# Performance work log

Hardware: AMD Instinct MI355X
Metric: run time of the kernel (lower is better)

Reference implementation:

```python
import jax, jax.numpy as jnp
import numpy as np
import math

B, LQ, LK = 4, 512, 512
D_MODEL, NHEAD, NLABELS = 512, 8, 8
D_Q = D_MODEL // NHEAD


def setup_inputs() -> dict:
    key = jax.random.key(0)
    ks = jax.random.split(key, 12)
    xavier = lambda k, shape: jax.random.uniform(
        k, shape, jnp.float32,
        -math.sqrt(6.0 / (shape[0] + shape[1])), math.sqrt(6.0 / (shape[0] + shape[1])))
    return {
        "q": jax.random.normal(ks[0], (B, LQ, D_MODEL), jnp.float32),
        "k": jax.random.normal(ks[1], (B, LK, D_MODEL), jnp.float32),
        "edge_mask": jax.random.randint(ks[2], (B, LQ, LK, NLABELS), 0, 2).astype(jnp.float32),
        "padding_mask": jax.random.randint(ks[3], (B, LQ, LK), 0, 2).astype(jnp.float32),
        "w_q_w": xavier(ks[4], (D_MODEL, D_MODEL)),
        "w_q_b": jnp.zeros((D_MODEL,), jnp.float32),
        "w_k": xavier(ks[5], (D_MODEL, D_MODEL)),
        "w_v": xavier(ks[6], (D_MODEL, D_MODEL)),
        "w_h_w": xavier(ks[7], (D_MODEL, D_MODEL)),
        "w_h_b": jnp.zeros((D_MODEL,), jnp.float32),
        "b_ks": xavier(ks[8], (NLABELS, D_Q)),
        "b_vs": xavier(ks[9], (NLABELS, D_Q)),
    }


def reference(q, k, edge_mask, padding_mask, w_q_w, w_q_b, w_k, w_v, w_h_w, w_h_b, b_ks, b_vs):
    sz_b, len_q, _ = q.shape
    len_k = k.shape[1]
    temp = np.power(D_Q, 0.5).astype(np.float32)

    # projections -> (nhead, B, L, d_q), matching torch permute(2,0,1,3)
    query = (q @ w_q_w.T + w_q_b).reshape(sz_b, len_q, NHEAD, D_Q).transpose(2, 0, 1, 3)
    key = (k @ w_k.T).reshape(sz_b, len_k, NHEAD, D_Q).transpose(2, 0, 1, 3)
    value = (k @ w_v.T).reshape(sz_b, len_k, NHEAD, D_Q).transpose(2, 0, 1, 3)

    # content scores + relation-bias scores
    qk = jnp.einsum('hbqd,hbkd->hbqk', query, key)
    key_rel = jnp.einsum('bqkl,ld->bqkd', edge_mask, b_ks)      # (B,Lq,Lk,d_q)
    qkr = jnp.einsum('hbqd,bqkd->hbqk', query, key_rel)
    output_attention_weights = (qk + qkr) / temp                # pre-mask, as returned by torch

    # mask where no edge label AND padding_mask==1
    relation_mask = (edge_mask.sum(-1) + (1.0 - padding_mask)) == 0  # (B,Lq,Lk)
    rm = relation_mask[None, :, :, :]                                # broadcast over heads
    attn = jnp.where(rm, -jnp.inf, output_attention_weights)
    attn = jax.nn.softmax(attn, axis=-1)
    attn = jnp.where(rm, 0.0, attn)

    # value aggregation: content + relation values
    qv = jnp.einsum('hbqk,hbkd->hbqd', attn, value)
    val_rel = jnp.einsum('bqkl,ld->bqkd', edge_mask, b_vs)
    qvr = jnp.einsum('hbqk,bqkd->hbqd', attn, val_rel)

    out = (qv + qvr).transpose(1, 2, 0, 3).reshape(sz_b, len_q, D_MODEL)
    out = out @ w_h_w.T + w_h_b
    return out, output_attention_weights.reshape(NHEAD * sz_b, len_q, len_k)
```

## Files before the change

kernel.cpp:

```cpp
#include <hip/hip_runtime.h>
#include <math.h>

#define NB 4
#define LQ 512
#define LK 512
#define DM 512
#define NH 8
#define DQ 64
#define NL 8
#define QT 32
#define PSTR 520

typedef short bf16x8 __attribute__((ext_vector_type(8)));
typedef _Float16 f16x8 __attribute__((ext_vector_type(8)));
typedef _Float16 f16x2 __attribute__((ext_vector_type(2)));
typedef float f32x4 __attribute__((ext_vector_type(4)));

__device__ __forceinline__ unsigned short f2bf(float x) {
    unsigned u = __float_as_uint(x);
    u += 0x7fff + ((u >> 16) & 1);
    return (unsigned short)(u >> 16);
}
__device__ __forceinline__ float bf2f(unsigned x) {
    return __uint_as_float(x << 16);
}
__device__ __forceinline__ unsigned short f2h(float x) {
    _Float16 h = (_Float16)x;
    return __builtin_bit_cast(unsigned short, h);
}
__device__ __forceinline__ void gld16(const void* g, void* l) {
    __builtin_amdgcn_global_load_lds(
        (const __attribute__((address_space(1))) void*)g,
        (__attribute__((address_space(3))) void*)l, 16, 0, 0);
}

#define WAITVM(N) asm volatile("s_waitcnt vmcnt(" #N ")" ::: "memory")
#define LGKM0()   asm volatile("s_waitcnt lgkmcnt(0)" ::: "memory")
#define BARR()    do { asm volatile("" ::: "memory"); \
                       __builtin_amdgcn_s_barrier();  \
                       asm volatile("" ::: "memory"); } while (0)

__global__ __launch_bounds__(256) void prep_kernel(
        const float* __restrict__ q,  const float* __restrict__ k,
        const float* __restrict__ wq, const float* __restrict__ wk,
        const float* __restrict__ wv, const float* __restrict__ wh,
        const float* __restrict__ em, const float* __restrict__ pad,
        unsigned short* __restrict__ qb,  unsigned short* __restrict__ kb,
        unsigned short* __restrict__ wqb, unsigned short* __restrict__ wkb,
        unsigned short* __restrict__ wvb, unsigned short* __restrict__ whb,
        unsigned short* __restrict__ Pk) {
    const int tid = threadIdx.x;
    const int y = blockIdx.y;
    if (y < 6) {
        const float* s; unsigned short* d; int n;
        switch (y) {
            case 0: s = q;  d = qb;  n = NB * LQ * DM; break;
            case 1: s = k;  d = kb;  n = NB * LK * DM; break;
            case 2: s = wq; d = wqb; n = DM * DM; break;
            case 3: s = wk; d = wkb; n = DM * DM; break;
            case 4: s = wv; d = wvb; n = DM * DM; break;
            default: s = wh; d = whb; n = DM * DM; break;
        }
        const int i = blockIdx.x * 256 + tid;
        if (i * 8 >= n) return;
        const float4* sv = (const float4*)s;
        const float4 a = sv[2 * (size_t)i], b = sv[2 * (size_t)i + 1];
        uint4 o;
        o.x = (unsigned)f2bf(a.x) | ((unsigned)f2bf(a.y) << 16);
        o.y = (unsigned)f2bf(a.z) | ((unsigned)f2bf(a.w) << 16);
        o.z = (unsigned)f2bf(b.x) | ((unsigned)f2bf(b.y) << 16);
        o.w = (unsigned)f2bf(b.z) | ((unsigned)f2bf(b.w) << 16);
        *(uint4*)(d + (size_t)i * 8) = o;
    } else {
        const int row = blockIdx.x * 4 + (tid >> 6);
        const int k0 = (tid & 63) * 8;
        const float* eb = em + ((size_t)row * LK + k0) * NL;
        const float4 pv0 = *(const float4*)(pad + (size_t)row * LK + k0);
        const float4 pv1 = *(const float4*)(pad + (size_t)row * LK + k0 + 4);
        const float pv[8] = {pv0.x, pv0.y, pv0.z, pv0.w, pv1.x, pv1.y, pv1.z, pv1.w};
        unsigned short outv[8];
#pragma unroll
        for (int kk = 0; kk < 8; ++kk) {
            const float4 v0 = *(const float4*)(eb + kk * 8);
            const float4 v1 = *(const float4*)(eb + kk * 8 + 4);
            unsigned b_ = 0;
            b_ |= (v0.x != 0.f) << 0; b_ |= (v0.y != 0.f) << 1;
            b_ |= (v0.z != 0.f) << 2; b_ |= (v0.w != 0.f) << 3;
            b_ |= (v1.x != 0.f) << 4; b_ |= (v1.y != 0.f) << 5;
            b_ |= (v1.z != 0.f) << 6; b_ |= (v1.w != 0.f) << 7;
            b_ |= (pv[kk] != 0.f) << 8;
            outv[kk] = (unsigned short)b_;
        }
        uint4 o;
        o.x = (unsigned)outv[0] | ((unsigned)outv[1] << 16);
        o.y = (unsigned)outv[2] | ((unsigned)outv[3] << 16);
        o.z = (unsigned)outv[4] | ((unsigned)outv[5] << 16);
        o.w = (unsigned)outv[6] | ((unsigned)outv[7] << 16);
        *(uint4*)(Pk + (size_t)row * LK + k0) = o;
    }
}

__device__ __forceinline__ void gemm64core(const unsigned short* __restrict__ Ag, int lda,
                                           const unsigned short* __restrict__ Bg, int ldb,
                                           short* As, short* Bs,
                                           f32x4 (&acc)[2][2]) {
    const int tid = threadIdx.x;
    const int wave = tid >> 6, lane = tid & 63;
    const int quad = lane >> 4, l16 = lane & 15;
    const int wr = wave >> 1, wc = wave & 1;
    const int r_ = tid >> 2, c_ = (tid & 3) * 8;
    const unsigned short* Ar = Ag + (size_t)r_ * lda + c_;
    const unsigned short* Br = Bg + (size_t)r_ * ldb + c_;
    gld16(Ar, (char*)As + wave * 1024);
    gld16(Br, (char*)Bs + wave * 1024);
#pragma unroll
    for (int s = 0; s < 16; ++s) {
        if (s < 15) {
            const int nb = (s + 1) & 1;
            gld16(Ar + (s + 1) * 32, (char*)As + nb * 4096 + wave * 1024);
            gld16(Br + (s + 1) * 32, (char*)Bs + nb * 4096 + wave * 1024);
            WAITVM(2);
        } else {
            WAITVM(0);
        }
        BARR();
        const int cb = s & 1;
        bf16x8 af[2], bf[2];
#pragma unroll
        for (int i = 0; i < 2; ++i)
            af[i] = *(const bf16x8*)&As[cb * 2048 + (wr * 32 + i * 16 + l16) * 32 + quad * 8];
#pragma unroll
        for (int j = 0; j < 2; ++j)
            bf[j] = *(const bf16x8*)&Bs[cb * 2048 + (wc * 32 + j * 16 + l16) * 32 + quad * 8];
#pragma unroll
        for (int i = 0; i < 2; ++i)
#pragma unroll
            for (int j = 0; j < 2; ++j)
                acc[i][j] = __builtin_amdgcn_mfma_f32_16x16x32_bf16(af[i], bf[j], acc[i][j], 0, 0, 0);
        BARR();
    }
}

__global__ __launch_bounds__(256) void proj_all(const unsigned short* __restrict__ qb,
                                                const unsigned short* __restrict__ kb,
                                                const unsigned short* __restrict__ wqb,
                                                const unsigned short* __restrict__ wkb,
                                                const unsigned short* __restrict__ wvb,
                                                const float* __restrict__ w_q_b,
                                                unsigned short* __restrict__ Qp,
                                                unsigned short* __restrict__ Kp,
                                                unsigned short* __restrict__ Vt) {
    __shared__ __align__(16) short As[2][64 * 32];
    __shared__ __align__(16) short Bs[2][64 * 32];
    const unsigned short* A; const unsigned short* W; const float* bias;
    unsigned short* C; int mode;
    switch (blockIdx.z) {
        case 0:  A = qb; W = wqb; bias = w_q_b;  C = Qp; mode = 0; break;
        case 1:  A = kb; W = wkb; bias = nullptr; C = Kp; mode = 0; break;
        default: A = kb; W = wvb; bias = nullptr; C = Vt; mode = 1; break;
    }
    f32x4 acc[2][2];
    const f32x4 zz = {0.f, 0.f, 0.f, 0.f};
#pragma unroll
    for (int i = 0; i < 2; ++i)
#pragma unroll
        for (int j = 0; j < 2; ++j) acc[i][j] = zz;
    const int m0 = blockIdx.x * 64, n0 = blockIdx.y * 64;
    gemm64core(A + (size_t)m0 * DM, DM, W + (size_t)n0 * DM, DM, &As[0][0], &Bs[0][0], acc);
    const int tid = threadIdx.x, wave = tid >> 6, lane = tid & 63;
    const int quad = lane >> 4, l16 = lane & 15;
    const int wr = wave >> 1, wc = wave & 1;
#pragma unroll
    for (int i = 0; i < 2; ++i)
#pragma unroll
        for (int r = 0; r < 4; ++r) {
            const int gm = m0 + wr * 32 + i * 16 + quad * 4 + r;
#pragma unroll
            for (int j = 0; j < 2; ++j) {
                const int gn = n0 + wc * 32 + j * 16 + l16;
                float v = acc[i][j][r];
                if (bias) v += bias[gn];
                if (mode == 0) C[(size_t)gm * DM + gn] = f2bf(v);
                else C[(size_t)(gm >> 9) * (DM * LK) + (size_t)gn * LK + (gm & 511)] = f2h(v);
            }
        }
}

#define STAGE_K(c, hb) do {                                                       \
    _Pragma("unroll")                                                             \
    for (int it_ = 0; it_ < 2; ++it_) {                                           \
        const int e_ = it_ * 512 + tid;                                           \
        const int kr_ = e_ >> 3, ch_ = e_ & 7;                                    \
        gld16(Kp + (size_t)(b * LK + (c) * 128 + kr_) * DM + h * DQ               \
                  + ((ch_ ^ (kr_ & 7)) * 8),                                      \
              (char*)&Kc[hb][0] + it_ * 8192 + wave * 1024);                      \
    } } while (0)

#define STAGE_V(vc, hb) do {                                                      \
    _Pragma("unroll")                                                             \
    for (int it_ = 0; it_ < 2; ++it_) {                                           \
        const int e_ = it_ * 512 + tid;                                           \
        const int dd_ = e_ >> 4, ch_ = e_ & 15;                                   \
        gld16(Vt + (size_t)(b * DM + h * DQ + dd_) * LK + (vc) * 128              \
                  + ((ch_ ^ (dd_ & 15)) * 8),                                     \
              (char*)&Kc[hb][0] + it_ * 8192 + wave * 1024);                      \
    } } while (0)

#define COMPUTE_K(c, hb) do {                                                     \
    _Pragma("unroll")                                                             \
    for (int kdi_ = 0; kdi_ < 2; ++kdi_) {                                        \
        const int krow_ = wave * 16 + l16;                                        \
        const int kch_ = (kdi_ * 4 + quad) ^ (krow_ & 7);                         \
        const bf16x8 bfv_ = *(const bf16x8*)&Kc[hb][krow_ * 64 + kch_ * 8];       \
        acc[c][0] = __builtin_amdgcn_mfma_f32_16x16x32_bf16(qf[0][kdi_], bfv_,    \
                                                            acc[c][0], 0, 0, 0); \
        acc[c][1] = __builtin_amdgcn_mfma_f32_16x16x32_bf16(qf[1][kdi_], bfv_,    \
                                                            acc[c][1], 0, 0, 0); \
    } } while (0)

#define COMPUTE_V(vc, hb) do {                                                    \
    _Pragma("unroll")                                                             \
    for (int kd_ = 0; kd_ < 128; kd_ += 32) {                                     \
        const int vrow_ = ni * 16 + l16;                                          \
        const int vch_ = ((kd_ >> 3) + quad) ^ (vrow_ & 15);                      \
        const f16x8 afv_ = *(const f16x8*)&Ps[(mi * 16 + l16) * PSTR              \
                                              + (vc) * 128 + kd_ + quad * 8];     \
        const f16x8 bfv_ = *(const f16x8*)&Kc[hb][vrow_ * 128 + vch_ * 8];        \
        oacc = __builtin_amdgcn_mfma_f32_16x16x32_f16(afv_, bfv_, oacc, 0, 0, 0); \
    } } while (0)

__global__ __launch_bounds__(512, 4) void attn_fused(
        const unsigned short* __restrict__ Qp,
        const unsigned short* __restrict__ Kp,
        const unsigned short* __restrict__ Vt,
        const unsigned short* __restrict__ Pk,
        const float* __restrict__ b_ks,
        const float* __restrict__ b_vs,
        float* __restrict__ weights,
        unsigned short* __restrict__ Hb) {
    __shared__ __align__(16) short Qs[QT * 64];
    __shared__ __align__(16) short Kc[2][128 * 64];
    __shared__ __align__(16) short Ps[QT * PSTR];
    __shared__ float svS[QT * NL];
    __shared__ float lutS[QT * 32];
    __shared__ float tS[QT * NL];
    __shared__ float redA[QT * 8];
    __shared__ float redB[QT * 8];

    const int tid = threadIdx.x, wave = tid >> 6, lane = tid & 63;
    const int quad = lane >> 4, l16 = lane & 15;
    const int q0 = blockIdx.x * QT;
    const int z = blockIdx.y, h = z >> 2, b = z & 3;

    const int srow = tid >> 4, sl = (tid >> 1) & 7, shalf = tid & 1;
    bf16x8 sq[4];
    {
        const unsigned short* qrow = Qp + (size_t)(b * LQ + q0 + srow) * DM + h * DQ + shalf * 32;
#pragma unroll
        for (int d0 = 0; d0 < 4; ++d0) sq[d0] = *(const bf16x8*)&qrow[d0 * 8];
    }

    if (tid < 256) {
        const int row = tid >> 3, ch = tid & 7;
        gld16(Qp + (size_t)(b * LQ + q0 + row) * DM + h * DQ + ((ch ^ (row & 7)) * 8),
              (char*)Qs + wave * 1024);
    }
    STAGE_K(0, 0);
    STAGE_K(1, 1);

    {
        const float* bk = b_ks + sl * DQ + shalf * 32;
        float s = 0.f;
#pragma unroll
        for (int d0 = 0; d0 < 4; ++d0)
#pragma unroll
            for (int j = 0; j < 8; ++j)
                s = fmaf(bf2f((unsigned short)sq[d0][j]), bk[d0 * 8 + j], s);
        s += __shfl_xor(s, 1, 64);
        if (shalf == 0) svS[srow * 8 + sl] = s;
    }

    f32x4 acc[4][2];
    const f32x4 zz = {0.f, 0.f, 0.f, 0.f};
#pragma unroll
    for (int c = 0; c < 4; ++c) { acc[c][0] = zz; acc[c][1] = zz; }
    bf16x8 qf[2][2];

    WAITVM(2); LGKM0(); BARR();
#pragma unroll
    for (int i = 0; i < 2; ++i)
#pragma unroll
        for (int kdi = 0; kdi < 2; ++kdi)
            qf[i][kdi] = *(const bf16x8*)&Qs[(i * 16 + l16) * 64
                                             + (((kdi * 4) + quad) ^ (l16 & 7)) * 8];
#pragma unroll
    for (int e2 = 0; e2 < 2; ++e2) {
        const int e = e2 * 512 + tid;
        const int row = e >> 5, idx = e & 31;
        const float* sp = &svS[row * 8 + ((idx & 16) ? 4 : 0)];
        float v = 0.f;
        v += (idx & 1) ? sp[0] : 0.f;
        v += (idx & 2) ? sp[1] : 0.f;
        v += (idx & 4) ? sp[2] : 0.f;
        v += (idx & 8) ? sp[3] : 0.f;
        lutS[e] = v;
    }
    COMPUTE_K(0, 0);
    LGKM0(); BARR();
    STAGE_K(2, 0);
    WAITVM(2); LGKM0(); BARR();
    COMPUTE_K(1, 1);
    LGKM0(); BARR();
    STAGE_K(3, 1);
    WAITVM(2); LGKM0(); BARR();
    COMPUTE_K(2, 0);
    LGKM0(); BARR();
    STAGE_V(0, 0);
    WAITVM(2); LGKM0(); BARR();
    COMPUTE_K(3, 1);
    LGKM0(); BARR();
    STAGE_V(1, 1);

#pragma unroll
    for (int i = 0; i < 2; ++i)
#pragma unroll
        for (int r = 0; r < 4; ++r) {
            const int row = i * 16 + quad * 4 + r;
            const int gq = q0 + row;
            const float* lrow = &lutS[row * 32];
            const unsigned short* prow = Pk + (size_t)(b * LQ + gq) * LK;
            float* wrow = weights + ((size_t)z * LQ + gq) * LK;
            float pm = -__builtin_inff();
#pragma unroll
            for (int c = 0; c < 4; ++c) {
                const int col = c * 128 + wave * 16 + l16;
                const unsigned w_ = prow[col];
                const float rel = lrow[w_ & 15u] + lrow[16 + ((w_ >> 4) & 15u)];
                const float wv = (acc[c][i][r] + rel) * 0.125f;
                wrow[col] = wv;
                const float m = ((w_ & 0x1FFu) == 0x100u) ? -__builtin_inff() : wv;
                acc[c][i][r] = m;
                pm = fmaxf(pm, m);
            }
#pragma unroll
            for (int o = 1; o < 16; o <<= 1) pm = fmaxf(pm, __shfl_xor(pm, o, 64));
            float ps = 0.f;
#pragma unroll
            for (int c = 0; c < 4; ++c) {
                const float e = __expf(acc[c][i][r] - pm);
                acc[c][i][r] = e;
                ps += e;
            }
#pragma unroll
            for (int o = 1; o < 16; o <<= 1) ps += __shfl_xor(ps, o, 64);
            if (l16 == 0) { redA[row * 8 + wave] = pm; redB[row * 8 + wave] = ps; }
        }
    LGKM0(); BARR();

#pragma unroll
    for (int i = 0; i < 2; ++i)
#pragma unroll
        for (int r = 0; r < 4; ++r) {
            const int row = i * 16 + quad * 4 + r;
            const f32x4 pa = *(const f32x4*)&redA[row * 8];
            const f32x4 pb = *(const f32x4*)&redA[row * 8 + 4];
            const f32x4 sa = *(const f32x4*)&redB[row * 8];
            const f32x4 sb = *(const f32x4*)&redB[row * 8 + 4];
            const float M = fmaxf(fmaxf(fmaxf(pa[0], pa[1]), fmaxf(pa[2], pa[3])),
                                  fmaxf(fmaxf(pb[0], pb[1]), fmaxf(pb[2], pb[3])));
            const float S = sa[0] * __expf(pa[0] - M) + sa[1] * __expf(pa[1] - M)
                          + sa[2] * __expf(pa[2] - M) + sa[3] * __expf(pa[3] - M)
                          + sb[0] * __expf(pb[0] - M) + sb[1] * __expf(pb[1] - M)
                          + sb[2] * __expf(pb[2] - M) + sb[3] * __expf(pb[3] - M);
            const float own = redA[row * 8 + wave];
            const float alpha = __expf(own - M) / S;
#pragma unroll
            for (int c = 0; c < 4; ++c) {
                const int col = c * 128 + wave * 16 + l16;
                Ps[row * PSTR + col] = (short)f2h(acc[c][i][r] * alpha);
            }
        }
    LGKM0(); BARR();

    {
        const int row = tid >> 4, l = (tid >> 1) & 7, half = tid & 1;
        const uint4* pw = (const uint4*)(Pk + (size_t)(b * LQ + q0 + row) * LK + half * 256);
        const uint4* aw = (const uint4*)&Ps[row * PSTR + half * 256];
        float tv = 0.f;
#pragma unroll 4
        for (int kk = 0; kk < 32; ++kk) {
            const uint4 wb = pw[kk];
            const uint4 av = aw[kk];
            const unsigned w4[4] = {wb.x, wb.y, wb.z, wb.w};
            const unsigned a4[4] = {av.x, av.y, av.z, av.w};
            f16x2 hacc = {(_Float16)0.f, (_Float16)0.f};
#pragma unroll
            for (int u = 0; u < 4; ++u) {
                const unsigned bits = (w4[u] >> l) & 0x10001u;
                const unsigned msk = bits * 0x3c00u;
                hacc += __builtin_bit_cast(f16x2, a4[u]) * __builtin_bit_cast(f16x2, msk);
            }
            tv += (float)hacc[0] + (float)hacc[1];
        }
        tv += __shfl_xor(tv, 1, 64);
        if (half == 0) tS[row * 8 + l] = tv;
    }

    f32x4 oacc = zz;
    const int mi = wave & 1, ni = wave >> 1;
    WAITVM(0); LGKM0(); BARR();
    COMPUTE_V(0, 0);
    BARR();
    STAGE_V(2, 0);
    WAITVM(2); LGKM0(); BARR();
    COMPUTE_V(1, 1);
    BARR();
    STAGE_V(3, 1);
    WAITVM(2); LGKM0(); BARR();
    COMPUTE_V(2, 0);
    WAITVM(0); LGKM0(); BARR();
    COMPUTE_V(3, 1);

    const int gd = ni * 16 + l16;
    float bvv[NL];
#pragma unroll
    for (int l = 0; l < NL; ++l) bvv[l] = b_vs[l * DQ + gd];
#pragma unroll
    for (int r = 0; r < 4; ++r) {
        const int row = mi * 16 + quad * 4 + r;
        const float* tp = &tS[row * 8];
        float o = oacc[r];
#pragma unroll
        for (int l = 0; l < NL; ++l) o = fmaf(tp[l], bvv[l], o);
        Hb[(size_t)(b * LQ + q0 + row) * DM + h * DQ + gd] = f2bf(o);
    }
}

__global__ __launch_bounds__(256) void outproj_mfma(const unsigned short* __restrict__ Hb,
                                                    const unsigned short* __restrict__ whb,
                                                    const float* __restrict__ bias,
                                                    float* __restrict__ C) {
    __shared__ __align__(16) short As[2][64 * 32];
    __shared__ __align__(16) short Bs[2][64 * 32];
    f32x4 acc[2][2];
    const f32x4 zz = {0.f, 0.f, 0.f, 0.f};
#pragma unroll
    for (int i = 0; i < 2; ++i)
#pragma unroll
        for (int j = 0; j < 2; ++j) acc[i][j] = zz;
    const int m0 = blockIdx.x * 64, n0 = blockIdx.y * 64;
    gemm64core(Hb + (size_t)m0 * DM, DM, whb + (size_t)n0 * DM, DM, &As[0][0], &Bs[0][0], acc);
    const int tid = threadIdx.x, wave = tid >> 6, lane = tid & 63;
    const int quad = lane >> 4, l16 = lane & 15;
    const int wr = wave >> 1, wc = wave & 1;
#pragma unroll
    for (int i = 0; i < 2; ++i)
#pragma unroll
        for (int r = 0; r < 4; ++r) {
            const int gm = m0 + wr * 32 + i * 16 + quad * 4 + r;
#pragma unroll
            for (int j = 0; j < 2; ++j) {
                const int gn = n0 + wc * 32 + j * 16 + l16;
                C[(size_t)gm * DM + gn] = acc[i][j][r] + bias[gn];
            }
        }
}

extern "C" void kernel_launch(void* const* d_in, const int* in_sizes, int n_in,
                              void* d_out, int out_size, void* d_ws, size_t ws_size,
                              hipStream_t stream) {
    const float* q     = (const float*)d_in[0];
    const float* k     = (const float*)d_in[1];
    const float* em    = (const float*)d_in[2];
    const float* pad   = (const float*)d_in[3];
    const float* w_q_w = (const float*)d_in[4];
    const float* w_q_b = (const float*)d_in[5];
    const float* w_k   = (const float*)d_in[6];
    const float* w_v   = (const float*)d_in[7];
    const float* w_h_w = (const float*)d_in[8];
    const float* w_h_b = (const float*)d_in[9];
    const float* b_ks  = (const float*)d_in[10];
    const float* b_vs  = (const float*)d_in[11];

    float* out     = (float*)d_out;
    float* weights = out + (size_t)NB * LQ * DM;

    char* ws = (char*)d_ws;
    unsigned short* qb  = (unsigned short*)(ws + 0);
    unsigned short* kb  = (unsigned short*)(ws + 2097152);
    unsigned short* wqb = (unsigned short*)(ws + 4194304);
    unsigned short* wkb = (unsigned short*)(ws + 4718592);
    unsigned short* wvb = (unsigned short*)(ws + 5242880);
    unsigned short* whb = (unsigned short*)(ws + 5767168);
    unsigned short* Qp  = (unsigned short*)(ws + 6291456);
    unsigned short* Kp  = (unsigned short*)(ws + 8388608);
    unsigned short* Vt  = (unsigned short*)(ws + 10485760);
    unsigned short* Hb  = (unsigned short*)(ws + 12582912);
    unsigned short* Pk  = (unsigned short*)(ws + 14680064);

    prep_kernel<<<dim3(512, 7), 256, 0, stream>>>(q, k, w_q_w, w_k, w_v, w_h_w,
                                                  em, pad, qb, kb, wqb, wkb, wvb, whb, Pk);
    proj_all<<<dim3(32, 8, 3), 256, 0, stream>>>(qb, kb, wqb, wkb, wvb, w_q_b, Qp, Kp, Vt);
    attn_fused<<<dim3(LQ / QT, 32), 512, 0, stream>>>(Qp, Kp, Vt, Pk, b_ks, b_vs, weights, Hb);
    outproj_mfma<<<dim3(32, 8), 256, 0, stream>>>(Hb, whb, w_h_b, out);
}
```

Before: 166.6 us.

## Fuse all stages into one cooperative persistent kernel with grid syncs

Replaces the four separate launches (convert/pack, projections, attention, output projection) with a single cooperative kernel of 512 blocks that runs each phase and separates them with grid-wide syncs. The attention body is factored into a device function that uses a shared-memory arena, and a templated GEMM routine is used for the projections, including a float-output mode for the final projection. The aim is to remove kernel launch gaps and tail effects between stages. In exchange each phase is tied to a fixed grid with grid barriers, and occupancy is limited by the 78 KB shared-memory footprint and 512-thread blocks. If the cooperative launch fails, the code falls back to the old multi-kernel path.

Result: slower. 373.8 us (+124.3%).

```diff
diff --git a/kernel.cpp b/kernel.cpp
--- a/kernel.cpp
+++ b/kernel.cpp
@@ -1,5 +1,8 @@
 #include <hip/hip_runtime.h>
+#include <hip/hip_cooperative_groups.h>
 #include <math.h>
+
+namespace cg = cooperative_groups;
 
 #define NB 4
 #define LQ 512
@@ -11,6 +14,16 @@
 #define QT 32
 #define PSTR 520
 
+#define SM_QS   0
+#define SM_KC   4096
+#define SM_PS   36864
+#define SM_SV   70144
+#define SM_LUT  71168
+#define SM_TS   75264
+#define SM_RA   76288
+#define SM_RB   77312
+#define SM_TOTAL 78336
+
 typedef short bf16x8 __attribute__((ext_vector_type(8)));
 typedef _Float16 f16x8 __attribute__((ext_vector_type(8)));
 typedef _Float16 f16x2 __attribute__((ext_vector_type(2)));
@@ -39,6 +52,432 @@
 #define BARR()    do { asm volatile("" ::: "memory"); \
                        __builtin_amdgcn_s_barrier();  \
                        asm volatile("" ::: "memory"); } while (0)
+
+
+__device__ __forceinline__ void conv_vec8(const float* __restrict__ s,
+                                          unsigned short* __restrict__ d, int i) {
+    const float4* sv = (const float4*)s;
+    const float4 a = sv[2 * (size_t)i], b = sv[2 * (size_t)i + 1];
+    uint4 o;
+    o.x = (unsigned)f2bf(a.x) | ((unsigned)f2bf(a.y) << 16);
+    o.y = (unsigned)f2bf(a.z) | ((unsigned)f2bf(a.w) << 16);
+    o.z = (unsigned)f2bf(b.x) | ((unsigned)f2bf(b.y) << 16);
+    o.w = (unsigned)f2bf(b.z) | ((unsigned)f2bf(b.w) << 16);
+    *(uint4*)(d + (size_t)i * 8) = o;
+}
+__device__ __forceinline__ void pack_pk(const float* __restrict__ em,
+                                        const float* __restrict__ pad,
+                                        unsigned short* __restrict__ Pk,
+                                        int row, int k0) {
+    const float* eb = em + ((size_t)row * LK + k0) * NL;
+    const float4 pv0 = *(const float4*)(pad + (size_t)row * LK + k0);
+    const float4 pv1 = *(const float4*)(pad + (size_t)row * LK + k0 + 4);
+    const float pv[8] = {pv0.x, pv0.y, pv0.z, pv0.w, pv1.x, pv1.y, pv1.z, pv1.w};
+    unsigned short outv[8];
+#pragma unroll
+    for (int kk = 0; kk < 8; ++kk) {
+        const float4 v0 = *(const float4*)(eb + kk * 8);
+        const float4 v1 = *(const float4*)(eb + kk * 8 + 4);
+        unsigned b_ = 0;
+        b_ |= (v0.x != 0.f) << 0; b_ |= (v0.y != 0.f) << 1;
+        b_ |= (v0.z != 0.f) << 2; b_ |= (v0.w != 0.f) << 3;
+        b_ |= (v1.x != 0.f) << 4; b_ |= (v1.y != 0.f) << 5;
+        b_ |= (v1.z != 0.f) << 6; b_ |= (v1.w != 0.f) << 7;
+        b_ |= (pv[kk] != 0.f) << 8;
+        outv[kk] = (unsigned short)b_;
+    }
+    uint4 o;
+    o.x = (unsigned)outv[0] | ((unsigned)outv[1] << 16);
+    o.y = (unsigned)outv[2] | ((unsigned)outv[3] << 16);
+    o.z = (unsigned)outv[4] | ((unsigned)outv[5] << 16);
+    o.w = (unsigned)outv[6] | ((unsigned)outv[7] << 16);
+    *(uint4*)(Pk + (size_t)row * LK + k0) = o;
+}
+
+template<int MODE>
+__device__ void gemm_macro(const unsigned short* __restrict__ Ag,
+                           const unsigned short* __restrict__ Bg,
+                           const float* __restrict__ bias,
+                           void* __restrict__ Cp,
+                           int m0, int n0p, char* smemc) {
+    short* As = (short*)(smemc);
+    short* Bs = (short*)(smemc + 8192);
+    const int tid = threadIdx.x;
+    const int wave = tid >> 6, lane = tid & 63;
+    const int quad = lane >> 4, l16 = lane & 15;
+    const int wl = wave & 3, wh = wave >> 2;
+    const int wr = wl >> 1, wc = wl & 1;
+    f32x4 acc[2][2];
+    const f32x4 zz = {0.f, 0.f, 0.f, 0.f};
+#pragma unroll
+    for (int i = 0; i < 2; ++i)
+#pragma unroll
+        for (int j = 0; j < 2; ++j) acc[i][j] = zz;
+    const int ar = lane >> 2, ac = (lane & 3) * 8;
+    const unsigned short* Arp = Ag + (size_t)(m0 + wave * 16 + ar) * DM + ac;
+    const unsigned short* Brp = Bg + (size_t)(n0p + wave * 16 + ar) * DM + ac;
+    if (wave < 4) gld16(Arp, (char*)As + wave * 1024);
+    gld16(Brp, (char*)Bs + wave * 1024);
+#pragma unroll
+    for (int s = 0; s < 16; ++s) {
+        if (s < 15) {
+            const int nb = (s + 1) & 1;
+            if (wave < 4) {
+                gld16(Arp + (s + 1) * 32, (char*)As + nb * 4096 + wave * 1024);
+                gld16(Brp + (s + 1) * 32, (char*)Bs + nb * 8192 + wave * 1024);
+                WAITVM(2);
+            } else {
+                gld16(Brp + (s + 1) * 32, (char*)Bs + nb * 8192 + wave * 1024);
+                WAITVM(1);
+            }
+        } else {
+            WAITVM(0);
+        }
+        BARR();
+        const int cb = s & 1;
+        bf16x8 af[2], bf[2];
+#pragma unroll
+        for (int i = 0; i < 2; ++i)
+            af[i] = *(const bf16x8*)&As[cb * 2048 + (wr * 32 + i * 16 + l16) * 32 + quad * 8];
+#pragma unroll
+        for (int j = 0; j < 2; ++j)
+            bf[j] = *(const bf16x8*)&Bs[cb * 4096 + (wh * 64 + wc * 32 + j * 16 + l16) * 32 + quad * 8];
+#pragma unroll
+        for (int i = 0; i < 2; ++i)
+#pragma unroll
+            for (int j = 0; j < 2; ++j)
+                acc[i][j] = __builtin_amdgcn_mfma_f32_16x16x32_bf16(af[i], bf[j], acc[i][j], 0, 0, 0);
+        BARR();
+    }
+#pragma unroll
+    for (int i = 0; i < 2; ++i)
+#pragma unroll
+        for (int r = 0; r < 4; ++r) {
+            const int gm = m0 + wr * 32 + i * 16 + quad * 4 + r;
+#pragma unroll
+            for (int j = 0; j < 2; ++j) {
+                const int gn = n0p + wh * 64 + wc * 32 + j * 16 + l16;
+                float v = acc[i][j][r];
+                if (MODE == 0) {
+                    if (bias) v += bias[gn];
+                    ((unsigned short*)Cp)[(size_t)gm * DM + gn] = f2bf(v);
+                } else if (MODE == 1) {
+                    ((unsigned short*)Cp)[(size_t)(gm >> 9) * (DM * LK)
+                                          + (size_t)gn * LK + (gm & 511)] = f2h(v);
+                } else {
+                    ((float*)Cp)[(size_t)gm * DM + gn] = v + bias[gn];
+                }
+            }
+        }
+}
+
+#define KC(hb) ((short*)(smemc + SM_KC + (hb) * 16384))
+
+#define STAGE_K(c, hb) do {                                                       \
+    _Pragma("unroll")                                                             \
+    for (int it_ = 0; it_ < 2; ++it_) {                                           \
+        const int e_ = it_ * 512 + tid;                                           \
+        const int kr_ = e_ >> 3, ch_ = e_ & 7;                                    \
+        gld16(Kp + (size_t)(b * LK + (c) * 128 + kr_) * DM + h * DQ               \
+                  + ((ch_ ^ (kr_ & 7)) * 8),                                      \
+              (char*)KC(hb) + it_ * 8192 + wave * 1024);                          \
+    } } while (0)
+
+#define STAGE_V(vc, hb) do {                                                      \
+    _Pragma("unroll")                                                             \
+    for (int it_ = 0; it_ < 2; ++it_) {                                           \
+        const int e_ = it_ * 512 + tid;                                           \
+        const int dd_ = e_ >> 4, ch_ = e_ & 15;                                   \
+        gld16(Vt + (size_t)(b * DM + h * DQ + dd_) * LK + (vc) * 128              \
+                  + ((ch_ ^ (dd_ & 15)) * 8),                                     \
+              (char*)KC(hb) + it_ * 8192 + wave * 1024);                          \
+    } } while (0)
+
+#define COMPUTE_K(c, hb) do {                                                     \
+    _Pragma("unroll")                                                             \
+    for (int kdi_ = 0; kdi_ < 2; ++kdi_) {                                        \
+        const int krow_ = wave * 16 + l16;                                        \
+        const int kch_ = (kdi_ * 4 + quad) ^ (krow_ & 7);                         \
+        const bf16x8 bfv_ = *(const bf16x8*)&KC(hb)[krow_ * 64 + kch_ * 8];       \
+        acc[c][0] = __builtin_amdgcn_mfma_f32_16x16x32_bf16(qf[0][kdi_], bfv_,    \
+                                                            acc[c][0], 0, 0, 0); \
+        acc[c][1] = __builtin_amdgcn_mfma_f32_16x16x32_bf16(qf[1][kdi_], bfv_,    \
+                                                            acc[c][1], 0, 0, 0); \
+    } } while (0)
+
+#define COMPUTE_V(vc, hb) do {                                                    \
+    _Pragma("unroll")                                                             \
+    for (int kd_ = 0; kd_ < 128; kd_ += 32) {                                     \
+        const int vrow_ = ni * 16 + l16;                                          \
+        const int vch_ = ((kd_ >> 3) + quad) ^ (vrow_ & 15);                      \
+        const f16x8 afv_ = *(const f16x8*)&Ps[(mi * 16 + l16) * PSTR              \
+                                              + (vc) * 128 + kd_ + quad * 8];     \
+        const f16x8 bfv_ = *(const f16x8*)&KC(hb)[vrow_ * 128 + vch_ * 8];        \
+        oacc = __builtin_amdgcn_mfma_f32_16x16x32_f16(afv_, bfv_, oacc, 0, 0, 0); \
+    } } while (0)
+
+__device__ void attn_body(char* smemc, const int xq, const int z,
+        const unsigned short* __restrict__ Qp,
+        const unsigned short* __restrict__ Kp,
+        const unsigned short* __restrict__ Vt,
+        const unsigned short* __restrict__ Pk,
+        const float* __restrict__ b_ks,
+        const float* __restrict__ b_vs,
+        float* __restrict__ weights,
+        unsigned short* __restrict__ Hb) {
+    short* Qs   = (short*)(smemc + SM_QS);
+    short* Ps   = (short*)(smemc + SM_PS);
+    float* svS  = (float*)(smemc + SM_SV);
+    float* lutS = (float*)(smemc + SM_LUT);
+    float* tS   = (float*)(smemc + SM_TS);
+    float* redA = (float*)(smemc + SM_RA);
+    float* redB = (float*)(smemc + SM_RB);
+
+    const int tid = threadIdx.x, wave = tid >> 6, lane = tid & 63;
+    const int quad = lane >> 4, l16 = lane & 15;
+    const int q0 = xq * QT;
+    const int h = z >> 2, b = z & 3;
+
+    const int srow = tid >> 4, sl = (tid >> 1) & 7, shalf = tid & 1;
+    bf16x8 sq[4];
+    {
+        const unsigned short* qrow = Qp + (size_t)(b * LQ + q0 + srow) * DM + h * DQ + shalf * 32;
+#pragma unroll
+        for (int d0 = 0; d0 < 4; ++d0) sq[d0] = *(const bf16x8*)&qrow[d0 * 8];
+    }
+
+    if (tid < 256) {
+        const int row = tid >> 3, ch = tid & 7;
+        gld16(Qp + (size_t)(b * LQ + q0 + row) * DM + h * DQ + ((ch ^ (row & 7)) * 8),
+              (char*)Qs + wave * 1024);
+    }
+    STAGE_K(0, 0);
+    STAGE_K(1, 1);
+
+    {
+        const float* bk = b_ks + sl * DQ + shalf * 32;
+        float s = 0.f;
+#pragma unroll
+        for (int d0 = 0; d0 < 4; ++d0)
+#pragma unroll
+            for (int j = 0; j < 8; ++j)
+                s = fmaf(bf2f((unsigned short)sq[d0][j]), bk[d0 * 8 + j], s);
+        s += __shfl_xor(s, 1, 64);
+        if (shalf == 0) svS[srow * 8 + sl] = s;
+    }
+
+    f32x4 acc[4][2];
+    const f32x4 zz = {0.f, 0.f, 0.f, 0.f};
+#pragma unroll
+    for (int c = 0; c < 4; ++c) { acc[c][0] = zz; acc[c][1] = zz; }
+    bf16x8 qf[2][2];
+
+    WAITVM(2); LGKM0(); BARR();
+#pragma unroll
+    for (int i = 0; i < 2; ++i)
+#pragma unroll
+        for (int kdi = 0; kdi < 2; ++kdi)
+            qf[i][kdi] = *(const bf16x8*)&Qs[(i * 16 + l16) * 64
+                                             + (((kdi * 4) + quad) ^ (l16 & 7)) * 8];
+#pragma unroll
+    for (int e2 = 0; e2 < 2; ++e2) {
+        const int e = e2 * 512 + tid;
+        const int row = e >> 5, idx = e & 31;
+        const float* sp = &svS[row * 8 + ((idx & 16) ? 4 : 0)];
+        float v = 0.f;
+        v += (idx & 1) ? sp[0] : 0.f;
+        v += (idx & 2) ? sp[1] : 0.f;
+        v += (idx & 4) ? sp[2] : 0.f;
+        v += (idx & 8) ? sp[3] : 0.f;
+        lutS[e] = v;
+    }
+    COMPUTE_K(0, 0);
+    LGKM0(); BARR();
+    STAGE_K(2, 0);
+    WAITVM(2); LGKM0(); BARR();
+    COMPUTE_K(1, 1);
+    LGKM0(); BARR();
+    STAGE_K(3, 1);
+    WAITVM(2); LGKM0(); BARR();
+    COMPUTE_K(2, 0);
+    LGKM0(); BARR();
+    STAGE_V(0, 0);
+    WAITVM(2); LGKM0(); BARR();
+    COMPUTE_K(3, 1);
+    LGKM0(); BARR();
+    STAGE_V(1, 1);
+
+#pragma unroll
+    for (int i = 0; i < 2; ++i)
+#pragma unroll
+        for (int r = 0; r < 4; ++r) {
+            const int row = i * 16 + quad * 4 + r;
+            const int gq = q0 + row;
+            const float* lrow = &lutS[row * 32];
+            const unsigned short* prow = Pk + (size_t)(b * LQ + gq) * LK;
+            float* wrow = weights + ((size_t)z * LQ + gq) * LK;
+            float pm = -__builtin_inff();
+#pragma unroll
+            for (int c = 0; c < 4; ++c) {
+                const int col = c * 128 + wave * 16 + l16;
+                const unsigned w_ = prow[col];
+                const float rel = lrow[w_ & 15u] + lrow[16 + ((w_ >> 4) & 15u)];
+                const float wv = (acc[c][i][r] + rel) * 0.125f;
+                wrow[col] = wv;
+                const float m = ((w_ & 0x1FFu) == 0x100u) ? -__builtin_inff() : wv;
+                acc[c][i][r] = m;
+                pm = fmaxf(pm, m);
+            }
+#pragma unroll
+            for (int o = 1; o < 16; o <<= 1) pm = fmaxf(pm, __shfl_xor(pm, o, 64));
+            float ps = 0.f;
+#pragma unroll
+            for (int c = 0; c < 4; ++c) {
+                const float e = __expf(acc[c][i][r] - pm);
+                acc[c][i][r] = e;
+                ps += e;
+            }
+#pragma unroll
+            for (int o = 1; o < 16; o <<= 1) ps += __shfl_xor(ps, o, 64);
+            if (l16 == 0) { redA[row * 8 + wave] = pm; redB[row * 8 + wave] = ps; }
+        }
+    LGKM0(); BARR();
+
+#pragma unroll
+    for (int i = 0; i < 2; ++i)
+#pragma unroll
+        for (int r = 0; r < 4; ++r) {
+            const int row = i * 16 + quad * 4 + r;
+            const f32x4 pa = *(const f32x4*)&redA[row * 8];
+            const f32x4 pb = *(const f32x4*)&redA[row * 8 + 4];
+            const f32x4 sa = *(const f32x4*)&redB[row * 8];
+            const f32x4 sb = *(const f32x4*)&redB[row * 8 + 4];
+            const float M = fmaxf(fmaxf(fmaxf(pa[0], pa[1]), fmaxf(pa[2], pa[3])),
+                                  fmaxf(fmaxf(pb[0], pb[1]), fmaxf(pb[2], pb[3])));
+            const float S = sa[0] * __expf(pa[0] - M) + sa[1] * __expf(pa[1] - M)
+                          + sa[2] * __expf(pa[2] - M) + sa[3] * __expf(pa[3] - M)
+                          + sb[0] * __expf(pb[0] - M) + sb[1] * __expf(pb[1] - M)
+                          + sb[2] * __expf(pb[2] - M) + sb[3] * __expf(pb[3] - M);
+            const float own = redA[row * 8 + wave];
+            const float alpha = __expf(own - M) / S;
+#pragma unroll
+            for (int c = 0; c < 4; ++c) {
+                const int col = c * 128 + wave * 16 + l16;
+                Ps[row * PSTR + col] = (short)f2h(acc[c][i][r] * alpha);
+            }
+        }
+    LGKM0(); BARR();
+
+    {
+        const int row = tid >> 4, l = (tid >> 1) & 7, half = tid & 1;
+        const uint4* pw = (const uint4*)(Pk + (size_t)(b * LQ + q0 + row) * LK + half * 256);
+        const uint4* aw = (const uint4*)&Ps[row * PSTR + half * 256];
+        float tv = 0.f;
+#pragma unroll 4
+        for (int kk = 0; kk < 32; ++kk) {
+            const uint4 wb = pw[kk];
+            const uint4 av = aw[kk];
+            const unsigned w4[4] = {wb.x, wb.y, wb.z, wb.w};
+            const unsigned a4[4] = {av.x, av.y, av.z, av.w};
+            f16x2 hacc = {(_Float16)0.f, (_Float16)0.f};
+#pragma unroll
+            for (int u = 0; u < 4; ++u) {
+                const unsigned bits = (w4[u] >> l) & 0x10001u;
+                const unsigned msk = bits * 0x3c00u;
+                hacc += __builtin_bit_cast(f16x2, a4[u]) * __builtin_bit_cast(f16x2, msk);
+            }
+            tv += (float)hacc[0] + (float)hacc[1];
+        }
+        tv += __shfl_xor(tv, 1, 64);
+        if (half == 0) tS[row * 8 + l] = tv;
+    }
+
+    f32x4 oacc = zz;
+    const int mi = wave & 1, ni = wave >> 1;
+    WAITVM(0); LGKM0(); BARR();
+    COMPUTE_V(0, 0);
+    BARR();
+    STAGE_V(2, 0);
+    WAITVM(2); LGKM0(); BARR();
+    COMPUTE_V(1, 1);
+    BARR();
+    STAGE_V(3, 1);
+    WAITVM(2); LGKM0(); BARR();
+    COMPUTE_V(2, 0);
+    WAITVM(0); LGKM0(); BARR();
+    COMPUTE_V(3, 1);
+
+    const int gd = ni * 16 + l16;
+    float bvv[NL];
+#pragma unroll
+    for (int l = 0; l < NL; ++l) bvv[l] = b_vs[l * DQ + gd];
+#pragma unroll
+    for (int r = 0; r < 4; ++r) {
+        const int row = mi * 16 + quad * 4 + r;
+        const float* tp = &tS[row * 8];
+        float o = oacc[r];
+#pragma unroll
+        for (int l = 0; l < NL; ++l) o = fmaf(tp[l], bvv[l], o);
+        Hb[(size_t)(b * LQ + q0 + row) * DM + h * DQ + gd] = f2bf(o);
+    }
+}
+
+__global__ __launch_bounds__(512, 4) void mega(
+        const float* __restrict__ q,  const float* __restrict__ k,
+        const float* __restrict__ em, const float* __restrict__ pad,
+        const float* __restrict__ w_q_w, const float* __restrict__ w_q_b,
+        const float* __restrict__ w_k,   const float* __restrict__ w_v,
+        const float* __restrict__ w_h_w, const float* __restrict__ w_h_b,
+        const float* __restrict__ b_ks,  const float* __restrict__ b_vs,
+        unsigned short* __restrict__ qb,  unsigned short* __restrict__ kb,
+        unsigned short* __restrict__ wqb, unsigned short* __restrict__ wkb,
+        unsigned short* __restrict__ wvb, unsigned short* __restrict__ whb,
+        unsigned short* __restrict__ Qp,  unsigned short* __restrict__ Kp,
+        unsigned short* __restrict__ Vt,  unsigned short* __restrict__ Hb,
+        unsigned short* __restrict__ Pk,
+        float* __restrict__ weights, float* __restrict__ out) {
+    __shared__ __align__(16) char smemc[SM_TOTAL];
+    cg::grid_group grid = cg::this_grid();
+    const int bid = blockIdx.x, tid = threadIdx.x;
+
+    {
+        for (int u = bid * 512 + tid; u < 393216; u += 262144) {
+            const float* s; unsigned short* d; int idx;
+            if (u < 131072)      { s = q; d = qb; idx = u; }
+            else if (u < 262144) { s = k; d = kb; idx = u - 131072; }
+            else {
+                const int v = u - 262144, w = v >> 15; idx = v & 32767;
+                switch (w) {
+                    case 0: s = w_q_w; d = wqb; break;
+                    case 1: s = w_k;   d = wkb; break;
+                    case 2: s = w_v;   d = wvb; break;
+                    default: s = w_h_w; d = whb; break;
+                }
+            }
+            conv_vec8(s, d, idx);
+        }
+        const int u2 = bid * 512 + tid;
+        if (u2 < 131072) pack_pk(em, pad, Pk, u2 >> 6, (u2 & 63) * 8);
+    }
+    grid.sync();
+
+    if (bid < 384) {
+        const int mat = bid >> 7, t = bid & 127;
+        const int m0 = (t >> 2) * 64, n0p = (t & 3) * 128;
+        if (mat == 0)      gemm_macro<0>(qb, wqb, w_q_b,  Qp, m0, n0p, smemc);
+        else if (mat == 1) gemm_macro<0>(kb, wkb, nullptr, Kp, m0, n0p, smemc);
+        else               gemm_macro<1>(kb, wvb, nullptr, Vt, m0, n0p, smemc);
+    }
+    grid.sync();
+
+    attn_body(smemc, bid & 15, bid >> 4, Qp, Kp, Vt, Pk, b_ks, b_vs, weights, Hb);
+    grid.sync();
+
+    if (bid < 128) {
+        const int m0 = (bid >> 2) * 64, n0p = (bid & 3) * 128;
+        gemm_macro<2>(Hb, whb, w_h_b, out, m0, n0p, smemc);
+    }
+}
 
 __global__ __launch_bounds__(256) void prep_kernel(
         const float* __restrict__ q,  const float* __restrict__ k,
@@ -63,40 +502,10 @@
         }
         const int i = blockIdx.x * 256 + tid;
         if (i * 8 >= n) return;
-        const float4* sv = (const float4*)s;
-        const float4 a = sv[2 * (size_t)i], b = sv[2 * (size_t)i + 1];
-        uint4 o;
-        o.x = (unsigned)f2bf(a.x) | ((unsigned)f2bf(a.y) << 16);
-        o.y = (unsigned)f2bf(a.z) | ((unsigned)f2bf(a.w) << 16);
-        o.z = (unsigned)f2bf(b.x) | ((unsigned)f2bf(b.y) << 16);
-        o.w = (unsigned)f2bf(b.z) | ((unsigned)f2bf(b.w) << 16);
-        *(uint4*)(d + (size_t)i * 8) = o;
+        conv_vec8(s, d, i);
     } else {
         const int row = blockIdx.x * 4 + (tid >> 6);
-        const int k0 = (tid & 63) * 8;
-        const float* eb = em + ((size_t)row * LK + k0) * NL;
-        const float4 pv0 = *(const float4*)(pad + (size_t)row * LK + k0);
-        const float4 pv1 = *(const float4*)(pad + (size_t)row * LK + k0 + 4);
-        const float pv[8] = {pv0.x, pv0.y, pv0.z, pv0.w, pv1.x, pv1.y, pv1.z, pv1.w};
-        unsigned short outv[8];
-#pragma unroll
-        for (int kk = 0; kk < 8; ++kk) {
-            const float4 v0 = *(const float4*)(eb + kk * 8);
-            const float4 v1 = *(const float4*)(eb + kk * 8 + 4);
-            unsigned b_ = 0;
-            b_ |= (v0.x != 0.f) << 0; b_ |= (v0.y != 0.f) << 1;
-            b_ |= (v0.z != 0.f) << 2; b_ |= (v0.w != 0.f) << 3;
-            b_ |= (v1.x != 0.f) << 4; b_ |= (v1.y != 0.f) << 5;
-            b_ |= (v1.z != 0.f) << 6; b_ |= (v1.w != 0.f) << 7;
-            b_ |= (pv[kk] != 0.f) << 8;
-            outv[kk] = (unsigned short)b_;
-        }
-        uint4 o;
-        o.x = (unsigned)outv[0] | ((unsigned)outv[1] << 16);
-        o.y = (unsigned)outv[2] | ((unsigned)outv[3] << 16);
-        o.z = (unsigned)outv[4] | ((unsigned)outv[5] << 16);
-        o.w = (unsigned)outv[6] | ((unsigned)outv[7] << 16);
-        *(uint4*)(Pk + (size_t)row * LK + k0) = o;
+        pack_pk(em, pad, Pk, row, (tid & 63) * 8);
     }
 }
 
@@ -186,49 +595,6 @@
         }
 }
 
-#define STAGE_K(c, hb) do {                                                       \
-    _Pragma("unroll")                                                             \
-    for (int it_ = 0; it_ < 2; ++it_) {                                           \
-        const int e_ = it_ * 512 + tid;                                           \
-        const int kr_ = e_ >> 3, ch_ = e_ & 7;                                    \
-        gld16(Kp + (size_t)(b * LK + (c) * 128 + kr_) * DM + h * DQ               \
-                  + ((ch_ ^ (kr_ & 7)) * 8),                                      \
-              (char*)&Kc[hb][0] + it_ * 8192 + wave * 1024);                      \
-    } } while (0)
-
-#define STAGE_V(vc, hb) do {                                                      \
-    _Pragma("unroll")                                                             \
-    for (int it_ = 0; it_ < 2; ++it_) {                                           \
-        const int e_ = it_ * 512 + tid;                                           \
-        const int dd_ = e_ >> 4, ch_ = e_ & 15;                                   \
-        gld16(Vt + (size_t)(b * DM + h * DQ + dd_) * LK + (vc) * 128              \
-                  + ((ch_ ^ (dd_ & 15)) * 8),                                     \
-              (char*)&Kc[hb][0] + it_ * 8192 + wave * 1024);                      \
-    } } while (0)
-
-#define COMPUTE_K(c, hb) do {                                                     \
-    _Pragma("unroll")                                                             \
-    for (int kdi_ = 0; kdi_ < 2; ++kdi_) {                                        \
-        const int krow_ = wave * 16 + l16;                                        \
-        const int kch_ = (kdi_ * 4 + quad) ^ (krow_ & 7);                         \
-        const bf16x8 bfv_ = *(const bf16x8*)&Kc[hb][krow_ * 64 + kch_ * 8];       \
-        acc[c][0] = __builtin_amdgcn_mfma_f32_16x16x32_bf16(qf[0][kdi_], bfv_,    \
-                                                            acc[c][0], 0, 0, 0); \
-        acc[c][1] = __builtin_amdgcn_mfma_f32_16x16x32_bf16(qf[1][kdi_], bfv_,    \
-                                                            acc[c][1], 0, 0, 0); \
-    } } while (0)
-
-#define COMPUTE_V(vc, hb) do {                                                    \
-    _Pragma("unroll")                                                             \
-    for (int kd_ = 0; kd_ < 128; kd_ += 32) {                                     \
-        const int vrow_ = ni * 16 + l16;                                          \
-        const int vch_ = ((kd_ >> 3) + quad) ^ (vrow_ & 15);                      \
-        const f16x8 afv_ = *(const f16x8*)&Ps[(mi * 16 + l16) * PSTR              \
-                                              + (vc) * 128 + kd_ + quad * 8];     \
-        const f16x8 bfv_ = *(const f16x8*)&Kc[hb][vrow_ * 128 + vch_ * 8];        \
-        oacc = __builtin_amdgcn_mfma_f32_16x16x32_f16(afv_, bfv_, oacc, 0, 0, 0); \
-    } } while (0)
-
 __global__ __launch_bounds__(512, 4) void attn_fused(
         const unsigned short* __restrict__ Qp,
         const unsigned short* __restrict__ Kp,
@@ -238,202 +604,8 @@
         const float* __restrict__ b_vs,
         float* __restrict__ weights,
         unsigned short* __restrict__ Hb) {
-    __shared__ __align__(16) short Qs[QT * 64];
-    __shared__ __align__(16) short Kc[2][128 * 64];
-    __shared__ __align__(16) short Ps[QT * PSTR];
-    __shared__ float svS[QT * NL];
-    __shared__ float lutS[QT * 32];
-    __shared__ float tS[QT * NL];
-    __shared__ float redA[QT * 8];
-    __shared__ float redB[QT * 8];
-
-    const int tid = threadIdx.x, wave = tid >> 6, lane = tid & 63;
-    const int quad = lane >> 4, l16 = lane & 15;
-    const int q0 = blockIdx.x * QT;
-    const int z = blockIdx.y, h = z >> 2, b = z & 3;
-
-    const int srow = tid >> 4, sl = (tid >> 1) & 7, shalf = tid & 1;
-    bf16x8 sq[4];
-    {
-        const unsigned short* qrow = Qp + (size_t)(b * LQ + q0 + srow) * DM + h * DQ + shalf * 32;
-#pragma unroll
-        for (int d0 = 0; d0 < 4; ++d0) sq[d0] = *(const bf16x8*)&qrow[d0 * 8];
-    }
-
-    if (tid < 256) {
-        const int row = tid >> 3, ch = tid & 7;
-        gld16(Qp + (size_t)(b * LQ + q0 + row) * DM + h * DQ + ((ch ^ (row & 7)) * 8),
-              (char*)Qs + wave * 1024);
-    }
-    STAGE_K(0, 0);
-    STAGE_K(1, 1);
-
-    {
-        const float* bk = b_ks + sl * DQ + shalf * 32;
-        float s = 0.f;
-#pragma unroll
-        for (int d0 = 0; d0 < 4; ++d0)
-#pragma unroll
-            for (int j = 0; j < 8; ++j)
-                s = fmaf(bf2f((unsigned short)sq[d0][j]), bk[d0 * 8 + j], s);
-        s += __shfl_xor(s, 1, 64);
-        if (shalf == 0) svS[srow * 8 + sl] = s;
-    }
-
-    f32x4 acc[4][2];
-    const f32x4 zz = {0.f, 0.f, 0.f, 0.f};
-#pragma unroll
-    for (int c = 0; c < 4; ++c) { acc[c][0] = zz; acc[c][1] = zz; }
-    bf16x8 qf[2][2];
-
-    WAITVM(2); LGKM0(); BARR();
-#pragma unroll
-    for (int i = 0; i < 2; ++i)
-#pragma unroll
-        for (int kdi = 0; kdi < 2; ++kdi)
-            qf[i][kdi] = *(const bf16x8*)&Qs[(i * 16 + l16) * 64
-                                             + (((kdi * 4) + quad) ^ (l16 & 7)) * 8];
-#pragma unroll
-    for (int e2 = 0; e2 < 2; ++e2) {
-        const int e = e2 * 512 + tid;
-        const int row = e >> 5, idx = e & 31;
-        const float* sp = &svS[row * 8 + ((idx & 16) ? 4 : 0)];
-        float v = 0.f;
-        v += (idx & 1) ? sp[0] : 0.f;
-        v += (idx & 2) ? sp[1] : 0.f;
-        v += (idx & 4) ? sp[2] : 0.f;
-        v += (idx & 8) ? sp[3] : 0.f;
-        lutS[e] = v;
-    }
-    COMPUTE_K(0, 0);
-    LGKM0(); BARR();
-    STAGE_K(2, 0);
-    WAITVM(2); LGKM0(); BARR();
-    COMPUTE_K(1, 1);
-    LGKM0(); BARR();
-    STAGE_K(3, 1);
-    WAITVM(2); LGKM0(); BARR();
-    COMPUTE_K(2, 0);
-    LGKM0(); BARR();
-    STAGE_V(0, 0);
-    WAITVM(2); LGKM0(); BARR();
-    COMPUTE_K(3, 1);
-    LGKM0(); BARR();
-    STAGE_V(1, 1);
-
-#pragma unroll
-    for (int i = 0; i < 2; ++i)
-#pragma unroll
-        for (int r = 0; r < 4; ++r) {
-            const int row = i * 16 + quad * 4 + r;
-            const int gq = q0 + row;
-            const float* lrow = &lutS[row * 32];
-            const unsigned short* prow = Pk + (size_t)(b * LQ + gq) * LK;
-            float* wrow = weights + ((size_t)z * LQ + gq) * LK;
-            float pm = -__builtin_inff();
-#pragma unroll
-            for (int c = 0; c < 4; ++c) {
-                const int col = c * 128 + wave * 16 + l16;
-                const unsigned w_ = prow[col];
-                const float rel = lrow[w_ & 15u] + lrow[16 + ((w_ >> 4) & 15u)];
-                const float wv = (acc[c][i][r] + rel) * 0.125f;
-                wrow[col] = wv;
-                const float m = ((w_ & 0x1FFu) == 0x100u) ? -__builtin_inff() : wv;
-                acc[c][i][r] = m;
-                pm = fmaxf(pm, m);
-            }
-#pragma unroll
-            for (int o = 1; o < 16; o <<= 1) pm = fmaxf(pm, __shfl_xor(pm, o, 64));
-            float ps = 0.f;
-#pragma unroll
-            for (int c = 0; c < 4; ++c) {
-                const float e = __expf(acc[c][i][r] - pm);
-                acc[c][i][r] = e;
-                ps += e;
-            }
-#pragma unroll
-            for (int o = 1; o < 16; o <<= 1) ps += __shfl_xor(ps, o, 64);
-            if (l16 == 0) { redA[row * 8 + wave] = pm; redB[row * 8 + wave] = ps; }
-        }
-    LGKM0(); BARR();
-
-#pragma unroll
-    for (int i = 0; i < 2; ++i)
-#pragma unroll
-        for (int r = 0; r < 4; ++r) {
-            const int row = i * 16 + quad * 4 + r;
-            const f32x4 pa = *(const f32x4*)&redA[row * 8];
-            const f32x4 pb = *(const f32x4*)&redA[row * 8 + 4];
-            const f32x4 sa = *(const f32x4*)&redB[row * 8];
-            const f32x4 sb = *(const f32x4*)&redB[row * 8 + 4];
-            const float M = fmaxf(fmaxf(fmaxf(pa[0], pa[1]), fmaxf(pa[2], pa[3])),
-                                  fmaxf(fmaxf(pb[0], pb[1]), fmaxf(pb[2], pb[3])));
-            const float S = sa[0] * __expf(pa[0] - M) + sa[1] * __expf(pa[1] - M)
-                          + sa[2] * __expf(pa[2] - M) + sa[3] * __expf(pa[3] - M)
-                          + sb[0] * __expf(pb[0] - M) + sb[1] * __expf(pb[1] - M)
-                          + sb[2] * __expf(pb[2] - M) + sb[3] * __expf(pb[3] - M);
-            const float own = redA[row * 8 + wave];
-            const float alpha = __expf(own - M) / S;
-#pragma unroll
-            for (int c = 0; c < 4; ++c) {
-                const int col = c * 128 + wave * 16 + l16;
-                Ps[row * PSTR + col] = (short)f2h(acc[c][i][r] * alpha);
-            }
-        }
-    LGKM0(); BARR();
-
-    {
-        const int row = tid >> 4, l = (tid >> 1) & 7, half = tid & 1;
-        const uint4* pw = (const uint4*)(Pk + (size_t)(b * LQ + q0 + row) * LK + half * 256);
-        const uint4* aw = (const uint4*)&Ps[row * PSTR + half * 256];
-        float tv = 0.f;
-#pragma unroll 4
-        for (int kk = 0; kk < 32; ++kk) {
-            const uint4 wb = pw[kk];
-            const uint4 av = aw[kk];
-            const unsigned w4[4] = {wb.x, wb.y, wb.z, wb.w};
-            const unsigned a4[4] = {av.x, av.y, av.z, av.w};
-            f16x2 hacc = {(_Float16)0.f, (_Float16)0.f};
-#pragma unroll
-            for (int u = 0; u < 4; ++u) {
-                const unsigned bits = (w4[u] >> l) & 0x10001u;
-                const unsigned msk = bits * 0x3c00u;
-                hacc += __builtin_bit_cast(f16x2, a4[u]) * __builtin_bit_cast(f16x2, msk);
-            }
-            tv += (float)hacc[0] + (float)hacc[1];
-        }
-        tv += __shfl_xor(tv, 1, 64);
-        if (half == 0) tS[row * 8 + l] = tv;
-    }
-
-    f32x4 oacc = zz;
-    const int mi = wave & 1, ni = wave >> 1;
-    WAITVM(0); LGKM0(); BARR();
-    COMPUTE_V(0, 0);
-    BARR();
-    STAGE_V(2, 0);
-    WAITVM(2); LGKM0(); BARR();
-    COMPUTE_V(1, 1);
-    BARR();
-    STAGE_V(3, 1);
-    WAITVM(2); LGKM0(); BARR();
-    COMPUTE_V(2, 0);
-    WAITVM(0); LGKM0(); BARR();
-    COMPUTE_V(3, 1);
-
-    const int gd = ni * 16 + l16;
-    float bvv[NL];
-#pragma unroll
-    for (int l = 0; l < NL; ++l) bvv[l] = b_vs[l * DQ + gd];
-#pragma unroll
-    for (int r = 0; r < 4; ++r) {
-        const int row = mi * 16 + quad * 4 + r;
-        const float* tp = &tS[row * 8];
-        float o = oacc[r];
-#pragma unroll
-        for (int l = 0; l < NL; ++l) o = fmaf(tp[l], bvv[l], o);
-        Hb[(size_t)(b * LQ + q0 + row) * DM + h * DQ + gd] = f2bf(o);
-    }
+    __shared__ __align__(16) char smemc[SM_TOTAL];
+    attn_body(smemc, blockIdx.x, blockIdx.y, Qp, Kp, Vt, Pk, b_ks, b_vs, weights, Hb);
 }
 
 __global__ __launch_bounds__(256) void outproj_mfma(const unsigned short* __restrict__ Hb,
@@ -498,9 +670,21 @@
     unsigned short* Hb  = (unsigned short*)(ws + 12582912);
     unsigned short* Pk  = (unsigned short*)(ws + 14680064);
 
-    prep_kernel<<<dim3(512, 7), 256, 0, stream>>>(q, k, w_q_w, w_k, w_v, w_h_w,
-                                                  em, pad, qb, kb, wqb, wkb, wvb, whb, Pk);
-    proj_all<<<dim3(32, 8, 3), 256, 0, stream>>>(qb, kb, wqb, wkb, wvb, w_q_b, Qp, Kp, Vt);
-    attn_fused<<<dim3(LQ / QT, 32), 512, 0, stream>>>(Qp, Kp, Vt, Pk, b_ks, b_vs, weights, Hb);
-    outproj_mfma<<<dim3(32, 8), 256, 0, stream>>>(Hb, whb, w_h_b, out);
-}
+    void* args[] = { (void*)&q, (void*)&k, (void*)&em, (void*)&pad,
+                     (void*)&w_q_w, (void*)&w_q_b, (void*)&w_k, (void*)&w_v,
+                     (void*)&w_h_w, (void*)&w_h_b, (void*)&b_ks, (void*)&b_vs,
+                     (void*)&qb, (void*)&kb, (void*)&wqb, (void*)&wkb,
+                     (void*)&wvb, (void*)&whb, (void*)&Qp, (void*)&Kp,
+                     (void*)&Vt, (void*)&Hb, (void*)&Pk,
+                     (void*)&weights, (void*)&out };
+    hipError_t e = hipLaunchCooperativeKernel(reinterpret_cast<void*>(mega),
+                                              dim3(512), dim3(512), args, 0, stream);
+    if (e != hipSuccess) {
+        (void)hipGetLastError();
+        prep_kernel<<<dim3(512, 7), 256, 0, stream>>>(q, k, w_q_w, w_k, w_v, w_h_w,
+                                                      em, pad, qb, kb, wqb, wkb, wvb, whb, Pk);
+        proj_all<<<dim3(32, 8, 3), 256, 0, stream>>>(qb, kb, wqb, wkb, wvb, w_q_b, Qp, Kp, Vt);
+        attn_fused<<<dim3(LQ / QT, 32), 512, 0, stream>>>(Qp, Kp, Vt, Pk, b_ks, b_vs, weights, Hb);
+        outproj_mfma<<<dim3(32, 8), 256, 0, stream>>>(Hb, whb, w_h_b, out);
+    }
+}
```
